# Kernel optimization log

Measured on AMD Instinct MI355X. Metric: run time of the kernel, lower is better.

## Reference

```python
import jax, jax.numpy as jnp
import numpy as np

H = 16          # n_heads
WIN = 256       # window_size
NEG_INF = -1e30 # finite stand-in for -inf to stay fp16/bf16 safe


def setup_inputs() -> dict:
    key = jax.random.key(0)
    ks = jax.random.split(key, 9)
    B, L, C = 2, 2048, 2048
    s = 0.02  # weight init scale
    inp = {
        "x": jax.random.normal(ks[0], (B, L, C), jnp.float32),
        "Wq": jax.random.normal(ks[1], (C, C), jnp.float32) * s,
        "bq": jnp.zeros((C,), jnp.float32),
        "Wk": jax.random.normal(ks[2], (C, C), jnp.float32) * s,
        "bk": jnp.zeros((C,), jnp.float32),
        "Wv": jax.random.normal(ks[3], (C, C), jnp.float32) * s,
        "bv": jnp.zeros((C,), jnp.float32),
        "Wo": jax.random.normal(ks[4], (C, C), jnp.float32) * s,
        "bo": jnp.zeros((C,), jnp.float32),
    }
    return inp


def _attn(x, Wq, bq, Wk, bk, Wv, bv, Wo, bo):
    B, L, C = x.shape
    D = C // H
    # torch Linear: y = x @ W.T + b
    q = (x @ Wq.T + bq).reshape(B, L, H, D).transpose(0, 2, 1, 3)  # (B,H,L,D)
    k = (x @ Wk.T + bk).reshape(B, L, H, D).transpose(0, 2, 1, 3)
    v = (x @ Wv.T + bv).reshape(B, L, H, D).transpose(0, 2, 1, 3)
    i = jnp.arange(L)[:, None]
    j = jnp.arange(L)[None, :]
    allowed = (j <= i) & (j > i - WIN)
    bias = jnp.where(allowed, 0.0, NEG_INF).astype(x.dtype)  # (L,L)
    scale = 1.0 / np.sqrt(D)
    attn = jnp.einsum('bhid,bhjd->bhij', q, k) + bias
    a = jax.nn.softmax(attn * scale, axis=-1)
    out = jnp.einsum('bhij,bhjd->bhid', a, v)  # (B,H,L,D)
    out = out.transpose(0, 2, 1, 3).reshape(B, L, C)
    return out @ Wo.T + bo  # dropout = identity (eval mode)


def reference(x, Wq, bq, Wk, bk, Wv, bv, Wo, bo):
    return _attn(x, Wq, bq, Wk, bk, Wv, bv, Wo, bo)
```

## Files before the change

kernel.cpp:

```cpp
#include <hip/hip_runtime.h>
#include <hip/hip_bf16.h>
#include <stdint.h>

typedef __bf16 bf16;
typedef __attribute__((ext_vector_type(8))) __bf16 bf16x8;
typedef __attribute__((ext_vector_type(8))) unsigned short u16x8;
typedef __attribute__((ext_vector_type(4))) float f32x4;

#define L_SEQ 2048
#define C_DIM 2048
#define NBATCH 2
#define M_ROWS (NBATCH * L_SEQ)
#define DH 128
#define NHEAD 16
#define WINSZ 256

__device__ __forceinline__ float san(float v, float s) {
    return ((__float_as_uint(v) & 0x7f800000u) == 0x7f800000u) ? s : v;
}

__device__ __forceinline__ bf16x8 pack8(float4 lo, float4 hi) {
    bf16x8 v;
    v[0] = (bf16)lo.x; v[1] = (bf16)lo.y; v[2] = (bf16)lo.z; v[3] = (bf16)lo.w;
    v[4] = (bf16)hi.x; v[5] = (bf16)hi.y; v[6] = (bf16)hi.z; v[7] = (bf16)hi.w;
    return v;
}

typedef const __attribute__((address_space(1))) void g_void;
typedef __attribute__((address_space(3))) void l_void;
__device__ __forceinline__ void glds16(const void* g, void* l) {
    __builtin_amdgcn_global_load_lds((g_void*)g, (l_void*)l, 16, 0, 0);
}

template <bool AF32, bool OUTF32>
__global__ __launch_bounds__(256)
void gemm_bt_bias(const void* __restrict__ Ap,
                  const float* __restrict__ W0, const float* __restrict__ b0, void* O0,
                  const float* __restrict__ W1, const float* __restrict__ b1, void* O1,
                  const float* __restrict__ W2, const float* __restrict__ b2, void* O2,
                  float snt)
{
    const int K = C_DIM, N = C_DIM;
    const float* W = W0; const float* bias = b0; void* Out = O0;
    if (blockIdx.z == 1)      { W = W1; bias = b1; Out = O1; }
    else if (blockIdx.z == 2) { W = W2; bias = b2; Out = O2; }

    __shared__ bf16 As[128 * 32];
    __shared__ bf16 Bs[128 * 32];

    const int tid  = threadIdx.x;
    const int lane = tid & 63;
    const int m0 = blockIdx.x * 128;
    const int n0 = blockIdx.y * 128;

    const int wave = tid >> 6;
    const int wm = (wave >> 1) * 64;
    const int wn = (wave & 1) * 64;

    const int srow = tid >> 2;
    const int scol = (tid & 3) * 8;

    f32x4 acc[4][4] = {};

    const int fr = lane & 15;
    const int fq = (lane >> 4) * 8;

    for (int k0 = 0; k0 < K; k0 += 32) {
        bf16x8 ra[2], rb[2];
        #pragma unroll
        for (int p = 0; p < 2; p++) {
            const size_t aoff = (size_t)(m0 + p * 64 + srow) * K + k0 + scol;
            if (AF32) {
                const float* A = (const float*)Ap;
                float4 lo = *(const float4*)(A + aoff);
                float4 hi = *(const float4*)(A + aoff + 4);
                ra[p] = pack8(lo, hi);
            } else {
                const bf16* A = (const bf16*)Ap;
                ra[p] = *(const bf16x8*)(A + aoff);
            }
            const size_t boff = (size_t)(n0 + p * 64 + srow) * K + k0 + scol;
            float4 wlo = *(const float4*)(W + boff);
            float4 whi = *(const float4*)(W + boff + 4);
            rb[p] = pack8(wlo, whi);
        }
        __syncthreads();
        #pragma unroll
        for (int p = 0; p < 2; p++) {
            *(bf16x8*)&As[(p * 64 + srow) * 32 + scol] = ra[p];
            *(bf16x8*)&Bs[(p * 64 + srow) * 32 + scol] = rb[p];
        }
        __syncthreads();

        bf16x8 af[4], bfr[4];
        #pragma unroll
        for (int s = 0; s < 4; s++)
            af[s] = *(const bf16x8*)&As[(wm + s * 16 + fr) * 32 + fq];
        #pragma unroll
        for (int s = 0; s < 4; s++)
            bfr[s] = *(const bf16x8*)&Bs[(wn + s * 16 + fr) * 32 + fq];
        #pragma unroll
        for (int sm = 0; sm < 4; sm++)
            #pragma unroll
            for (int sn = 0; sn < 4; sn++)
                acc[sm][sn] = __builtin_amdgcn_mfma_f32_16x16x32_bf16(af[sm], bfr[sn], acc[sm][sn], 0, 0, 0);
    }

    const int r0 = (lane >> 4) * 4;
    const int cn = lane & 15;
    #pragma unroll
    for (int sn = 0; sn < 4; sn++) {
        const int n = n0 + wn + sn * 16 + cn;
        const float bv = bias[n];
        #pragma unroll
        for (int sm = 0; sm < 4; sm++) {
            const int m = m0 + wm + sm * 16 + r0;
            #pragma unroll
            for (int r = 0; r < 4; r++) {
                const float v = san(acc[sm][sn][r] + bv, snt);
                if (OUTF32) ((float*)Out)[(size_t)(m + r) * N + n] = v;
                else        ((bf16*)Out)[(size_t)(m + r) * N + n] = (bf16)v;
            }
        }
    }
}

template <bool OUTF32>
__global__ __launch_bounds__(256)
void gemm_bb_bias(const bf16* __restrict__ A,
                  const bf16* __restrict__ W0, const float* __restrict__ b0, void* O0,
                  const bf16* __restrict__ W1, const float* __restrict__ b1, void* O1,
                  const bf16* __restrict__ W2, const float* __restrict__ b2, void* O2,
                  float snt)
{
    const int K = C_DIM, N = C_DIM;
    const bf16* W = W0; const float* bias = b0; void* Out = O0;
    if (blockIdx.z == 1)      { W = W1; bias = b1; Out = O1; }
    else if (blockIdx.z == 2) { W = W2; bias = b2; Out = O2; }

    __shared__ bf16 As[128 * 32];
    __shared__ bf16 Bs[128 * 32];

    const int tid  = threadIdx.x;
    const int lane = tid & 63;
    const int wv   = tid >> 6;

    int wg = blockIdx.x + (int)gridDim.x * blockIdx.y;
    wg = (wg & 7) * 64 + (wg >> 3);
    const int m0 = (wg & 31) * 128;
    const int n0 = (wg >> 5) * 128;

    const int grow = tid >> 2;
    const int gcol = (tid & 3) * 8;
    char* const asw = (char*)As + wv * 1024;
    char* const bsw = (char*)Bs + wv * 1024;

    f32x4 acc[4][4] = {};

    const int fr = lane & 15;
    const int fq = (lane >> 4) * 8;
    const int wm = (wv >> 1) * 64;
    const int wn = (wv & 1) * 64;

    const bf16* arow = A + (size_t)(m0 + grow) * K + gcol;
    const bf16* brow = W + (size_t)(n0 + grow) * K + gcol;

    for (int k0 = 0; k0 < K; k0 += 32) {
        __syncthreads();
        glds16(arow + k0,               asw);
        glds16(arow + k0 + 64 * K,      asw + 4096);
        glds16(brow + k0,               bsw);
        glds16(brow + k0 + 64 * K,      bsw + 4096);
        __syncthreads();

        bf16x8 af[4], bfr[4];
        #pragma unroll
        for (int s = 0; s < 4; s++)
            af[s] = *(const bf16x8*)&As[(wm + s * 16 + fr) * 32 + fq];
        #pragma unroll
        for (int s = 0; s < 4; s++)
            bfr[s] = *(const bf16x8*)&Bs[(wn + s * 16 + fr) * 32 + fq];
        #pragma unroll
        for (int sm = 0; sm < 4; sm++)
            #pragma unroll
            for (int sn = 0; sn < 4; sn++)
                acc[sm][sn] = __builtin_amdgcn_mfma_f32_16x16x32_bf16(af[sm], bfr[sn], acc[sm][sn], 0, 0, 0);
    }

    const int r0 = (lane >> 4) * 4;
    const int cn = lane & 15;
    #pragma unroll
    for (int sn = 0; sn < 4; sn++) {
        const int n = n0 + wn + sn * 16 + cn;
        const float bv = bias[n];
        #pragma unroll
        for (int sm = 0; sm < 4; sm++) {
            const int m = m0 + wm + sm * 16 + r0;
            #pragma unroll
            for (int r = 0; r < 4; r++) {
                const float v = san(acc[sm][sn][r] + bv, snt);
                if (OUTF32) ((float*)Out)[(size_t)(m + r) * N + n] = v;
                else        ((bf16*)Out)[(size_t)(m + r) * N + n] = (bf16)v;
            }
        }
    }
}

__global__ __launch_bounds__(256)
void cvt_f32_bf16(const float* __restrict__ s0, bf16* __restrict__ d0,
                  const float* __restrict__ s1, bf16* __restrict__ d1,
                  const float* __restrict__ s2, bf16* __restrict__ d2,
                  const float* __restrict__ s3, bf16* __restrict__ d3,
                  const float* __restrict__ s4, bf16* __restrict__ d4)
{
    const float* s; bf16* d; int n;
    switch (blockIdx.y) {
        case 0:  s = s0; d = d0; n = M_ROWS * C_DIM; break;
        case 1:  s = s1; d = d1; n = C_DIM * C_DIM; break;
        case 2:  s = s2; d = d2; n = C_DIM * C_DIM; break;
        case 3:  s = s3; d = d3; n = C_DIM * C_DIM; break;
        default: s = s4; d = d4; n = C_DIM * C_DIM; break;
    }
    const int nv = n >> 3;
    const int stride = (int)gridDim.x * 256;
    for (int i = blockIdx.x * 256 + threadIdx.x; i < nv; i += stride) {
        const float4 lo = *(const float4*)(s + (size_t)i * 8);
        const float4 hi = *(const float4*)(s + (size_t)i * 8 + 4);
        *(bf16x8*)(d + (size_t)i * 8) = pack8(lo, hi);
    }
}

#define SWZK(r, byteoff) ((((r) * 256) + (byteoff)) ^ (((r) & 7) << 4))
#define SWZV(d, byteoff) ((((d) * 128) + (byteoff)) ^ (((((d) & 7) ^ (((d) >> 3) & 7))) << 4))
#define SWZP(r, byteoff) ((((r) * 128) + (byteoff)) ^ (((r) & 7) << 4))

__global__ __launch_bounds__(256)
void swa_attn(const bf16* __restrict__ Q, const bf16* __restrict__ Kp,
              const bf16* __restrict__ V, bf16* __restrict__ Oattn, float snt)
{
    __shared__ bf16 Ks[64 * 128];
    __shared__ bf16 Vt[128 * 64];
    __shared__ bf16 Ps[64 * 64];

    const int tid  = threadIdx.x;
    const int lane = tid & 63;
    const int w    = tid >> 6;
    const int q0 = blockIdx.x * 64;
    const int h  = blockIdx.y;
    const int b  = blockIdx.z;
    const size_t base = (size_t)b * L_SEQ * C_DIM + (size_t)h * DH;

    const int fr  = lane & 15;
    const int g   = lane >> 4;
    const int fq8 = g * 8;

    bf16x8 qf[4];
    {
        const bf16* qrow = Q + base + (size_t)(q0 + w * 16 + fr) * C_DIM;
        #pragma unroll
        for (int kk = 0; kk < 4; kk++)
            qf[kk] = *(const bf16x8*)(qrow + kk * 32 + fq8);
    }

    const int rl0 = g * 4;
    const int ig  = q0 + w * 16 + rl0;
    const float scale = 0.08838834764831845f;

    float m_run[4], l_run[4];
    #pragma unroll
    for (int r = 0; r < 4; r++) { m_run[r] = -1e30f; l_run[r] = 0.0f; }
    f32x4 Oacc[8] = {};

    const int krr = tid >> 4;
    const int kcc = (tid & 15) * 8;
    const int vc  = tid & 15;
    const int vd0 = vc * 8;
    const int vpb = tid >> 4;

    for (int kb = 0; kb < 5; kb++) {
        const int s = q0 - 256 + kb * 64;
        if (s < 0) continue;

        __syncthreads();

        #pragma unroll
        for (int p = 0; p < 4; p++) {
            const int r = p * 16 + krr;
            const uint4 kv = *(const uint4*)(Kp + base + (size_t)(s + r) * C_DIM + kcc);
            *(uint4*)((char*)Ks + SWZK(r, kcc * 2)) = kv;
        }
        #pragma unroll
        for (int it = 0; it < 2; it++) {
            const int p = vpb + it * 16;
            const bf16* vr = V + base + (size_t)(s + 2 * p) * C_DIM + vd0;
            const u16x8 va = *(const u16x8*)vr;
            const u16x8 vb = *(const u16x8*)(vr + C_DIM);
            #pragma unroll
            for (int j = 0; j < 8; j++) {
                const uint32_t val = (uint32_t)va[j] | ((uint32_t)vb[j] << 16);
                *(uint32_t*)((char*)Vt + SWZV(vd0 + j, 4 * p)) = val;
            }
        }
        __syncthreads();

        f32x4 sacc[4] = {};
        __builtin_amdgcn_s_setprio(1);
        #pragma unroll
        for (int kk = 0; kk < 4; kk++) {
            #pragma unroll
            for (int t = 0; t < 4; t++) {
                const bf16x8 kf = *(const bf16x8*)((char*)Ks + SWZK(t * 16 + fr, (kk * 32 + fq8) * 2));
                sacc[t] = __builtin_amdgcn_mfma_f32_16x16x32_bf16(qf[kk], kf, sacc[t], 0, 0, 0);
            }
        }
        __builtin_amdgcn_s_setprio(0);

        float alpha[4];
        #pragma unroll
        for (int r = 0; r < 4; r++) {
            const int iq = ig + r;
            float p4[4];
            float bm = -1e30f;
            #pragma unroll
            for (int t = 0; t < 4; t++) {
                const int j = s + t * 16 + fr;
                const bool allow = (j <= iq) && (j > iq - WINSZ);
                p4[t] = allow ? sacc[t][r] * scale : -1e30f;
                bm = fmaxf(bm, p4[t]);
            }
            bm = fmaxf(bm, __shfl_xor(bm, 1, 64));
            bm = fmaxf(bm, __shfl_xor(bm, 2, 64));
            bm = fmaxf(bm, __shfl_xor(bm, 4, 64));
            bm = fmaxf(bm, __shfl_xor(bm, 8, 64));
            const float m_new = fmaxf(m_run[r], bm);
            alpha[r] = __expf(m_run[r] - m_new);
            m_run[r] = m_new;
            float ps = 0.0f;
            #pragma unroll
            for (int t = 0; t < 4; t++) {
                const float e = (p4[t] > -1e29f) ? __expf(p4[t] - m_new) : 0.0f;
                p4[t] = e;
                ps += e;
            }
            ps += __shfl_xor(ps, 1, 64);
            ps += __shfl_xor(ps, 2, 64);
            ps += __shfl_xor(ps, 4, 64);
            ps += __shfl_xor(ps, 8, 64);
            l_run[r] = l_run[r] * alpha[r] + ps;

            const int prow = w * 16 + rl0 + r;
            #pragma unroll
            for (int t = 0; t < 4; t++)
                *(bf16*)((char*)Ps + SWZP(prow, (t * 16 + fr) * 2)) = (bf16)p4[t];
        }

        #pragma unroll
        for (int t = 0; t < 8; t++)
            #pragma unroll
            for (int r = 0; r < 4; r++)
                Oacc[t][r] *= alpha[r];

        __builtin_amdgcn_s_setprio(1);
        #pragma unroll
        for (int kk = 0; kk < 2; kk++) {
            const bf16x8 pa = *(const bf16x8*)((char*)Ps + SWZP(w * 16 + fr, (kk * 32 + fq8) * 2));
            #pragma unroll
            for (int t = 0; t < 8; t++) {
                const bf16x8 vf = *(const bf16x8*)((char*)Vt + SWZV(t * 16 + fr, (kk * 32 + fq8) * 2));
                Oacc[t] = __builtin_amdgcn_mfma_f32_16x16x32_bf16(pa, vf, Oacc[t], 0, 0, 0);
            }
        }
        __builtin_amdgcn_s_setprio(0);
    }

    bf16* ob = Oattn + base;
    #pragma unroll
    for (int r = 0; r < 4; r++) {
        const float inv_l = 1.0f / l_run[r];
        const size_t ro = (size_t)(q0 + w * 16 + rl0 + r) * C_DIM;
        #pragma unroll
        for (int t = 0; t < 8; t++)
            ob[ro + t * 16 + fr] = (bf16)san(Oacc[t][r] * inv_l, snt);
    }
}

__global__ void fill_signal(float* out, int n, float v) {
    for (int i = blockIdx.x * blockDim.x + threadIdx.x; i < n; i += gridDim.x * blockDim.x)
        out[i] = v;
}

extern "C" void kernel_launch(void* const* d_in, const int* in_sizes, int n_in,
                              void* d_out, int out_size, void* d_ws, size_t ws_size,
                              hipStream_t stream) {
    const size_t sz      = (size_t)M_ROWS * C_DIM;
    const size_t wsz     = (size_t)C_DIM * C_DIM;
    const size_t bfbytes = sz * sizeof(bf16);
    const size_t FASTNEED = 3 * sz * sizeof(bf16) + 4 * wsz * sizeof(bf16);

    const int expn[9] = {8388608, 4194304, 2048, 4194304, 2048,
                         4194304, 2048, 4194304, 2048};
    float sig = 0.0f;
    if (n_in != 9) sig = 1100.0f;
    else {
        for (int i = 0; i < 9; i++)
            if (in_sizes[i] != expn[i]) { sig = 1200.0f + 100.0f * i; break; }
    }
    if (sig == 0.0f && out_size != (int)sz) sig = 2100.0f;
    if (sig == 0.0f && ws_size < 2 * bfbytes) sig = 3000.0f + 10.0f * (float)(ws_size >> 20);
    if (sig != 0.0f) {
        fill_signal<<<512, 256, 0, stream>>>((float*)d_out, (int)sz, sig);
        return;
    }

    const float* x  = (const float*)d_in[0];
    const float* Wq = (const float*)d_in[1];
    const float* bq = (const float*)d_in[2];
    const float* Wk = (const float*)d_in[3];
    const float* bk = (const float*)d_in[4];
    const float* Wv = (const float*)d_in[5];
    const float* bv = (const float*)d_in[6];
    const float* Wo = (const float*)d_in[7];
    const float* bo = (const float*)d_in[8];

    if (ws_size >= FASTNEED) {
        bf16* xbf = (bf16*)d_ws;
        bf16* kws = xbf + sz;
        bf16* vws = kws + sz;
        bf16* wqb = vws + sz;
        bf16* wkb = wqb + wsz;
        bf16* wvb = wkb + wsz;
        bf16* wob = wvb + wsz;
        bf16*  qscr  = (bf16*)d_out;
        float* out32 = (float*)d_out;

        cvt_f32_bf16<<<dim3(2048, 5), 256, 0, stream>>>(
            x, xbf, Wq, wqb, Wk, wkb, Wv, wvb, Wo, wob);

        gemm_bb_bias<false><<<dim3(32, 16, 3), 256, 0, stream>>>(
            xbf, wqb, bq, (void*)qscr, wkb, bk, (void*)kws,
            wvb, bv, (void*)vws, 111.0f);

        swa_attn<<<dim3(L_SEQ / 64, NHEAD, NBATCH), 256, 0, stream>>>(
            qscr, kws, vws, xbf, 222.0f);

        gemm_bb_bias<true><<<dim3(32, 16, 1), 256, 0, stream>>>(
            xbf, wob, bo, (void*)out32, wob, bo, (void*)out32,
            wob, bo, (void*)out32, 444.0f);
    } else {
        bf16*  kws   = (bf16*)d_ws;
        bf16*  vws   = kws + sz;
        bf16*  qscr  = (bf16*)d_out;
        float* out32 = (float*)d_out;

        gemm_bt_bias<true, false><<<dim3(32, 16, 3), 256, 0, stream>>>(
            (const void*)x, Wq, bq, (void*)qscr, Wk, bk, (void*)kws,
            Wv, bv, (void*)vws, 111.0f);

        swa_attn<<<dim3(L_SEQ / 64, NHEAD, NBATCH), 256, 0, stream>>>(
            qscr, kws, vws, qscr, 222.0f);

        hipMemcpyAsync(kws, qscr, bfbytes, hipMemcpyDeviceToDevice, stream);

        gemm_bt_bias<false, true><<<dim3(32, 16, 1), 256, 0, stream>>>(
            (const void*)kws, Wo, bo, (void*)out32, Wo, bo, (void*)out32,
            Wo, bo, (void*)out32, 444.0f);
    }
}
```

Measured before the change: 386.6 us.

## Replace 128x128 GEMM with 256x256 double-buffered ping-pong pipelined GEMM

```diff
diff --git a/kernel.cpp b/kernel.cpp
--- a/kernel.cpp
+++ b/kernel.cpp
@@ -125,85 +125,161 @@
     }
 }
 
+__device__ __forceinline__ void phase_mid() {
+    asm volatile("" ::: "memory");
+    __builtin_amdgcn_s_barrier();
+    asm volatile("s_waitcnt lgkmcnt(0)" ::: "memory");
+    __builtin_amdgcn_sched_barrier(0);
+    __builtin_amdgcn_s_setprio(1);
+}
+__device__ __forceinline__ void phase_end() {
+    __builtin_amdgcn_s_setprio(0);
+    asm volatile("" ::: "memory");
+    __builtin_amdgcn_s_barrier();
+}
+
+#define LOADA(d, qm) do {                                                     \
+    char* s_ = lds + (d) * 65536 + ahalf * 16384;                             \
+    _Pragma("unroll") for (int sm = 0; sm < 4; sm++)                          \
+    _Pragma("unroll") for (int kk = 0; kk < 2; kk++) {                        \
+        const int row_ = (qm) * 64 + sm * 16 + fr;                            \
+        afr[sm][kk] = *(const bf16x8*)(s_ + row_ * 128 +                      \
+                        (((kk * 4 + g) ^ (row_ & 7)) << 4));                  \
+    } } while (0)
+
+#define LOADB(d, qn, arr) do {                                                \
+    char* s_ = lds + (d) * 65536 + 32768 + bhalf * 16384;                     \
+    _Pragma("unroll") for (int sn = 0; sn < 2; sn++)                          \
+    _Pragma("unroll") for (int kk = 0; kk < 2; kk++) {                        \
+        const int row_ = brow0 + (qn) * 32 + sn * 16 + fr;                    \
+        arr[sn][kk] = *(const bf16x8*)(s_ + row_ * 128 +                      \
+                        (((kk * 4 + g) ^ (row_ & 7)) << 4));                  \
+    } } while (0)
+
+#define MFMA16(qm, qn, arr) do {                                              \
+    _Pragma("unroll") for (int kk = 0; kk < 2; kk++)                          \
+    _Pragma("unroll") for (int sm = 0; sm < 4; sm++)                          \
+    _Pragma("unroll") for (int sn = 0; sn < 2; sn++)                          \
+        acc[(qm) * 4 + sm][(qn) * 2 + sn] =                                   \
+            __builtin_amdgcn_mfma_f32_16x16x32_bf16(afr[sm][kk], arr[sn][kk], \
+                acc[(qm) * 4 + sm][(qn) * 2 + sn], 0, 0, 0);                  \
+    } while (0)
+
 template <bool OUTF32>
-__global__ __launch_bounds__(256)
-void gemm_bb_bias(const bf16* __restrict__ A,
-                  const bf16* __restrict__ W0, const float* __restrict__ b0, void* O0,
-                  const bf16* __restrict__ W1, const float* __restrict__ b1, void* O1,
-                  const bf16* __restrict__ W2, const float* __restrict__ b2, void* O2,
-                  float snt)
+__global__ __launch_bounds__(512, 2)
+void gemm_256(const bf16* __restrict__ A,
+              const bf16* __restrict__ W0, const float* __restrict__ b0, void* O0,
+              const bf16* __restrict__ W1, const float* __restrict__ b1, void* O1,
+              const bf16* __restrict__ W2, const float* __restrict__ b2, void* O2,
+              float snt)
 {
     const int K = C_DIM, N = C_DIM;
+    const int NT = K / 64;
     const bf16* W = W0; const float* bias = b0; void* Out = O0;
     if (blockIdx.z == 1)      { W = W1; bias = b1; Out = O1; }
     else if (blockIdx.z == 2) { W = W2; bias = b2; Out = O2; }
 
-    __shared__ bf16 As[128 * 32];
-    __shared__ bf16 Bs[128 * 32];
+    __shared__ __attribute__((aligned(16))) char lds[131072];
 
     const int tid  = threadIdx.x;
     const int lane = tid & 63;
-    const int wv   = tid >> 6;
-
-    int wg = blockIdx.x + (int)gridDim.x * blockIdx.y;
-    wg = (wg & 7) * 64 + (wg >> 3);
-    const int m0 = (wg & 31) * 128;
-    const int n0 = (wg >> 5) * 128;
-
-    const int grow = tid >> 2;
-    const int gcol = (tid & 3) * 8;
-    char* const asw = (char*)As + wv * 1024;
-    char* const bsw = (char*)Bs + wv * 1024;
-
-    f32x4 acc[4][4] = {};
-
+    const int w    = tid >> 6;
+
+    int id = blockIdx.x + (int)gridDim.x * blockIdx.y;
+    id = (id & 7) * 16 + (id >> 3);
+    const int m0 = (id & 15) * 256;
+    const int n0 = (id >> 4) * 256;
+
+    const int wm = (w >> 2) * 128;
+    const int wn = (w & 3) * 64;
     const int fr = lane & 15;
-    const int fq = (lane >> 4) * 8;
-    const int wm = (wv >> 1) * 64;
-    const int wn = (wv & 1) * 64;
-
-    const bf16* arow = A + (size_t)(m0 + grow) * K + gcol;
-    const bf16* brow = W + (size_t)(n0 + grow) * K + gcol;
-
-    for (int k0 = 0; k0 < K; k0 += 32) {
-        __syncthreads();
-        glds16(arow + k0,               asw);
-        glds16(arow + k0 + 64 * K,      asw + 4096);
-        glds16(brow + k0,               bsw);
-        glds16(brow + k0 + 64 * K,      bsw + 4096);
-        __syncthreads();
-
-        bf16x8 af[4], bfr[4];
-        #pragma unroll
-        for (int s = 0; s < 4; s++)
-            af[s] = *(const bf16x8*)&As[(wm + s * 16 + fr) * 32 + fq];
-        #pragma unroll
-        for (int s = 0; s < 4; s++)
-            bfr[s] = *(const bf16x8*)&Bs[(wn + s * 16 + fr) * 32 + fq];
-        #pragma unroll
-        for (int sm = 0; sm < 4; sm++)
-            #pragma unroll
-            for (int sn = 0; sn < 4; sn++)
-                acc[sm][sn] = __builtin_amdgcn_mfma_f32_16x16x32_bf16(af[sm], bfr[sn], acc[sm][sn], 0, 0, 0);
-    }
-
+    const int g  = lane >> 4;
+    const int ahalf = w >> 2;
+    const int bhalf = (w >> 1) & 1;
+    const int brow0 = (w & 1) * 64;
+
+    const int srow  = tid >> 3;
+    const int scol  = (((tid & 7) ^ (srow & 7)) * 8);
+    const int wvoff = (tid >> 6) * 1024;
+
+    f32x4 acc[8][4] = {};
+    bf16x8 afr[4][2], b0r[2][2], b1r[2][2];
+
+    #define STAGE_A(t, h) do {                                                \
+        const int d_ = (t) & 1;                                               \
+        const int tc_ = (t) < NT ? (t) : NT - 1;                              \
+        const bf16* src_ = A + (size_t)(m0 + (h) * 128 + srow) * K            \
+                             + tc_ * 64 + scol;                               \
+        char* dst_ = lds + d_ * 65536 + (h) * 16384 + wvoff;                  \
+        glds16(src_, dst_);                                                   \
+        glds16(src_ + (size_t)64 * K, dst_ + 8192);                           \
+    } while (0)
+
+    #define STAGE_B(t, h) do {                                                \
+        const int d_ = (t) & 1;                                               \
+        const int tc_ = (t) < NT ? (t) : NT - 1;                              \
+        const bf16* src_ = W + (size_t)(n0 + (h) * 128 + srow) * K            \
+                             + tc_ * 64 + scol;                               \
+        char* dst_ = lds + d_ * 65536 + 32768 + (h) * 16384 + wvoff;          \
+        glds16(src_, dst_);                                                   \
+        glds16(src_ + (size_t)64 * K, dst_ + 8192);                           \
+    } while (0)
+
+    STAGE_B(0, 0); STAGE_B(0, 1); STAGE_A(0, 0); STAGE_A(0, 1);
+    STAGE_B(1, 0); STAGE_B(1, 1);
+    asm volatile("s_waitcnt vmcnt(4)" ::: "memory");
+    asm volatile("" ::: "memory");
+    __builtin_amdgcn_s_barrier();
+
+    #pragma unroll 1
+    for (int i = 0; i < NT / 2; i++) {
+        const int t1 = 2 * i + 1, t2 = 2 * i + 2, t3 = 2 * i + 3;
+        LOADA(0, 0); LOADB(0, 0, b0r);
+        STAGE_A(t1, 0);
+        phase_mid(); MFMA16(0, 0, b0r); phase_end();
+        LOADB(0, 1, b1r);
+        STAGE_A(t1, 1);
+        phase_mid(); MFMA16(0, 1, b1r); phase_end();
+        LOADA(0, 1);
+        STAGE_B(t2, 0);
+        phase_mid(); MFMA16(1, 1, b1r); phase_end();
+        STAGE_B(t2, 1);
+        asm volatile("s_waitcnt vmcnt(4)" ::: "memory");
+        phase_mid(); MFMA16(1, 0, b0r); phase_end();
+        LOADA(1, 0); LOADB(1, 0, b0r);
+        STAGE_A(t2, 0);
+        phase_mid(); MFMA16(0, 0, b0r); phase_end();
+        LOADB(1, 1, b1r);
+        STAGE_A(t2, 1);
+        phase_mid(); MFMA16(0, 1, b1r); phase_end();
+        LOADA(1, 1);
+        STAGE_B(t3, 0);
+        phase_mid(); MFMA16(1, 1, b1r); phase_end();
+        STAGE_B(t3, 1);
+        asm volatile("s_waitcnt vmcnt(4)" ::: "memory");
+        phase_mid(); MFMA16(1, 0, b0r); phase_end();
+    }
+    asm volatile("s_waitcnt vmcnt(0)" ::: "memory");
+
+    const int cn = lane & 15;
     const int r0 = (lane >> 4) * 4;
-    const int cn = lane & 15;
     #pragma unroll
-    for (int sn = 0; sn < 4; sn++) {
-        const int n = n0 + wn + sn * 16 + cn;
+    for (int sn2 = 0; sn2 < 4; sn2++) {
+        const int n = n0 + wn + sn2 * 16 + cn;
         const float bv = bias[n];
         #pragma unroll
-        for (int sm = 0; sm < 4; sm++) {
-            const int m = m0 + wm + sm * 16 + r0;
+        for (int sm2 = 0; sm2 < 8; sm2++) {
+            const int m = m0 + wm + sm2 * 16 + r0;
             #pragma unroll
             for (int r = 0; r < 4; r++) {
-                const float v = san(acc[sm][sn][r] + bv, snt);
+                const float v = san(acc[sm2][sn2][r] + bv, snt);
                 if (OUTF32) ((float*)Out)[(size_t)(m + r) * N + n] = v;
                 else        ((bf16*)Out)[(size_t)(m + r) * N + n] = (bf16)v;
             }
         }
     }
+    #undef STAGE_A
+    #undef STAGE_B
 }
 
 __global__ __launch_bounds__(256)
@@ -436,14 +512,14 @@
         cvt_f32_bf16<<<dim3(2048, 5), 256, 0, stream>>>(
             x, xbf, Wq, wqb, Wk, wkb, Wv, wvb, Wo, wob);
 
-        gemm_bb_bias<false><<<dim3(32, 16, 3), 256, 0, stream>>>(
+        gemm_256<false><<<dim3(16, 8, 3), 512, 0, stream>>>(
             xbf, wqb, bq, (void*)qscr, wkb, bk, (void*)kws,
             wvb, bv, (void*)vws, 111.0f);
 
         swa_attn<<<dim3(L_SEQ / 64, NHEAD, NBATCH), 256, 0, stream>>>(
             qscr, kws, vws, xbf, 222.0f);
 
-        gemm_bb_bias<true><<<dim3(32, 16, 1), 256, 0, stream>>>(
+        gemm_256<true><<<dim3(16, 8, 1), 512, 0, stream>>>(
             xbf, wob, bo, (void*)out32, wob, bo, (void*)out32,
             wob, bo, (void*)out32, 444.0f);
     } else {
```

Result: faster. 359.8 us (-6.9%).
